# Kernel optimization log

Hardware: AMD Instinct MI355X
Metric: run time of the kernel (lower is better)

Reference implementation:

```python
import jax, jax.numpy as jnp
import numpy as np

K_STEPS = 10
ALPHA = 0.9
N_NODES = 16384
N_CLASSES = 64
N_EDGES = 524288


def setup_inputs() -> dict:
    key = jax.random.key(0)
    k1, k2, k3 = jax.random.split(key, 3)
    masked_y_true = jax.random.normal(k1, (N_NODES, N_CLASSES), dtype=jnp.float32)
    K = jax.random.normal(k2, (N_NODES, N_NODES), dtype=jnp.float32)
    edge_index = jax.random.randint(k3, (2, N_EDGES), 0, N_NODES, dtype=jnp.int32)
    return {"masked_y_true": masked_y_true, "K": K, "edge_index": edge_index}


def reference(masked_y_true, K, edge_index):
    src, dst = edge_index[0], edge_index[1]
    # DAD normalization: w_e = deg(src)^-1/2 * deg(dst)^-1/2
    deg = jnp.zeros((N_NODES,), jnp.float32).at[dst].add(1.0)
    dinv = jax.lax.rsqrt(jnp.maximum(deg, 1.0))
    w = dinv[src] * dinv[dst]  # [E]

    def spmm(x):
        # A @ x with A in edge-list form (static sparsity, reused each step)
        return jax.ops.segment_sum(w[:, None] * x[src], dst, num_segments=N_NODES)

    def prop_step(_, y):
        return ALPHA * spmm(y) + (1.0 - ALPHA) * y

    y = jax.lax.fori_loop(0, K_STEPS, prop_step, masked_y_true)
    y = K @ y
    y = jax.lax.fori_loop(0, K_STEPS, prop_step, y)
    return y
```

## Files before the change

### kernel.cpp

```cpp
#include <hip/hip_runtime.h>

#define NN 16384
#define NC 64
#define NE 524288
#define ALPHA 0.9f
#define KSTEPS 10

typedef _Float16 f16;
typedef _Float16 f16x4 __attribute__((ext_vector_type(4)));
typedef _Float16 f16x8 __attribute__((ext_vector_type(8)));
typedef float f32x4 __attribute__((ext_vector_type(4)));
typedef int i32x16 __attribute__((ext_vector_type(16)));

#define MEMB   asm volatile("" ::: "memory")
#define SCHED0 __builtin_amdgcn_sched_barrier(0)

__global__ __launch_bounds__(256) void deg_kernel(const int* __restrict__ dst,
                                                  unsigned* __restrict__ deg) {
    int e = blockIdx.x * 256 + threadIdx.x;
    atomicAdd(&deg[dst[e]], 1u);
}

__global__ __launch_bounds__(1024) void scan_kernel(const unsigned* __restrict__ deg,
                                                    float* __restrict__ dinv,
                                                    unsigned* __restrict__ rowoff,
                                                    unsigned* __restrict__ cursor) {
    __shared__ unsigned part[1024];
    const int t = threadIdx.x;
    const int base = t * 16;
    unsigned local[16];
    unsigned s = 0;
    #pragma unroll
    for (int i = 0; i < 16; ++i) {
        local[i] = s;
        s += (deg[base + i] + 15u) & ~15u;
    }
    part[t] = s;
    __syncthreads();
    for (int off = 1; off < 1024; off <<= 1) {
        unsigned v = (t >= off) ? part[t - off] : 0u;
        __syncthreads();
        part[t] += v;
        __syncthreads();
    }
    const unsigned ex = (t == 0) ? 0u : part[t - 1];
    #pragma unroll
    for (int i = 0; i < 16; ++i) {
        unsigned ro = ex + local[i];
        rowoff[base + i] = ro;
        cursor[base + i] = ro;
        unsigned d = deg[base + i];
        dinv[base + i] = rsqrtf(fmaxf((float)d, 1.0f));
    }
    if (t == 1023) rowoff[NN] = part[1023];
}

__global__ __launch_bounds__(256) void fill_kernel(const int* __restrict__ src,
                                                   const int* __restrict__ dst,
                                                   const float* __restrict__ dinv,
                                                   unsigned* __restrict__ cursor,
                                                   int2* __restrict__ csr) {
    int e = blockIdx.x * 256 + threadIdx.x;
    int s = src[e], d = dst[e];
    float w = dinv[s] * dinv[d];
    unsigned p = atomicAdd(&cursor[d], 1u);
    csr[p] = make_int2(s, __float_as_int(w));
}

__global__ __launch_bounds__(256) void prop_kernel(const float* __restrict__ x,
                                                   float* __restrict__ y,
                                                   const unsigned* __restrict__ rowoff,
                                                   const int* __restrict__ csr) {
    const int lane = threadIdx.x & 63;
    const int bid = blockIdx.x;
    const int n = __builtin_amdgcn_readfirstlane(((bid & 7) << 11) + ((bid >> 3) << 2)
                                                 + (threadIdx.x >> 6));
    const unsigned beg = rowoff[n];
    const unsigned np = (rowoff[n + 1] - beg) >> 4;
    float acc0 = 0.f, acc1 = 0.f;
    if (np) {
        i32x16 e0 = *(const i32x16*)(csr + 2 * beg);
        i32x16 e1 = *(const i32x16*)(csr + 2 * beg + 16);
        float xv0[8], xv1[8];
        #pragma unroll
        for (int j = 0; j < 8; ++j) xv0[j] = x[(unsigned)e0[2 * j] * 64u + lane];
        #pragma unroll
        for (int j = 0; j < 8; ++j) xv1[j] = x[(unsigned)e1[2 * j] * 64u + lane];
        for (unsigned p = 1; p < np; ++p) {
            const i32x16 f0 = *(const i32x16*)(csr + 2 * (beg + p * 16));
            const i32x16 f1 = *(const i32x16*)(csr + 2 * (beg + p * 16) + 16);
            #pragma unroll
            for (int j = 0; j < 8; ++j) {
                const float w = __int_as_float(e0[2 * j + 1]);
                if (j & 1) acc1 = fmaf(w, xv0[j], acc1);
                else       acc0 = fmaf(w, xv0[j], acc0);
            }
            #pragma unroll
            for (int j = 0; j < 8; ++j) xv0[j] = x[(unsigned)f0[2 * j] * 64u + lane];
            #pragma unroll
            for (int j = 0; j < 8; ++j) {
                const float w = __int_as_float(e1[2 * j + 1]);
                if (j & 1) acc1 = fmaf(w, xv1[j], acc1);
                else       acc0 = fmaf(w, xv1[j], acc0);
            }
            #pragma unroll
            for (int j = 0; j < 8; ++j) xv1[j] = x[(unsigned)f1[2 * j] * 64u + lane];
            e0 = f0; e1 = f1;
        }
        #pragma unroll
        for (int j = 0; j < 8; ++j) {
            const float w = __int_as_float(e0[2 * j + 1]);
            if (j & 1) acc1 = fmaf(w, xv0[j], acc1);
            else       acc0 = fmaf(w, xv0[j], acc0);
        }
        #pragma unroll
        for (int j = 0; j < 8; ++j) {
            const float w = __int_as_float(e1[2 * j + 1]);
            if (j & 1) acc1 = fmaf(w, xv1[j], acc1);
            else       acc0 = fmaf(w, xv1[j], acc0);
        }
    }
    y[n * 64 + lane] = ALPHA * (acc0 + acc1) + (1.0f - ALPHA) * x[n * 64 + lane];
}

__global__ __launch_bounds__(256) void ysplit_kernel(const float* __restrict__ y,
                                                     f16* __restrict__ yhT,
                                                     f16* __restrict__ ylT) {
    __shared__ f16 hb[64][72];
    __shared__ f16 lb[64][72];
    const int t = threadIdx.x;
    const int b = blockIdx.x;
    const int kl = t >> 2;
    const int cq = (t & 3) * 16;
    #pragma unroll
    for (int i = 0; i < 4; ++i) {
        float4 v = *(const float4*)&y[(size_t)(b * 64 + kl) * 64 + cq + i * 4];
        float vv[4] = {v.x, v.y, v.z, v.w};
        #pragma unroll
        for (int j = 0; j < 4; ++j) {
            int c = cq + i * 4 + j;
            f16 h = (f16)vv[j];
            float r = vv[j] - (float)h;
            hb[c][kl] = h;
            lb[c][kl] = (f16)r;
        }
    }
    __syncthreads();
    const int c = t >> 2;
    const int kq = (t & 3) * 16;
    #pragma unroll
    for (int s2 = 0; s2 < 2; ++s2) {
        int slot = (kq >> 3) + s2;
        int dslot = slot ^ (c & 7);
        f16x8 hv, lv;
        #pragma unroll
        for (int j = 0; j < 8; ++j) { hv[j] = hb[c][kq + s2 * 8 + j]; lv[j] = lb[c][kq + s2 * 8 + j]; }
        *(f16x8*)&yhT[(size_t)c * NN + b * 64 + dslot * 8] = hv;
        *(f16x8*)&ylT[(size_t)c * NN + b * 64 + dslot * 8] = lv;
    }
}

__device__ inline void gload16(const void* g, void* l) {
    __builtin_amdgcn_global_load_lds((const __attribute__((address_space(1))) void*)g,
                                     (__attribute__((address_space(3))) void*)l, 16, 0, 0);
}

#define AH_OFF 0
#define AL_OFF 16384
#define YP_OFF 32768

template <bool SLAB>
__global__ __launch_bounds__(256, 2) void gemm_kernel(const float* __restrict__ A,
                                                      const f16* __restrict__ yhT,
                                                      const f16* __restrict__ ylT,
                                                      float* __restrict__ z) {
    __shared__ char lds[65536];
    const int t = threadIdx.x;
    const int w = t >> 6;
    const int l = t & 63;
    const size_t row0 = (size_t)blockIdx.x * 128;
    const int kbase = blockIdx.y * 2048;
    const int stag = (blockIdx.x + blockIdx.y * 4) & 31;

    f32x4 acc[2][4];
    #pragma unroll
    for (int m = 0; m < 2; ++m)
        #pragma unroll
        for (int n = 0; n < 4; ++n)
            acc[m][n] = (f32x4){0.f, 0.f, 0.f, 0.f};

    const int arow_l = w * 4 + (l >> 4);
    const int acol = (l & 15) * 4;
    const int ycr = l >> 3;
    const int yco = (l & 7) * 8;

    float4 aA[8], aB[8];

    auto tmap = [&](int tile) { return (stag + tile) & 31; };

    auto loadA = [&](float4 (&dst)[8], int tile) {
        const int kt = kbase + tmap(tile) * 64;
        #pragma unroll
        for (int i = 0; i < 8; ++i)
            dst[i] = *(const float4*)&A[(row0 + i * 16 + arow_l) * 16384 + kt + acol];
    };
    auto issueY = [&](int tile, int cur) {
        const int kt = kbase + tmap(tile) * 64;
        #pragma unroll
        for (int j = 0; j < 2; ++j) {
            const int i = 2 * w + j;
            gload16(yhT + (size_t)(i * 8 + ycr) * NN + kt + yco,
                    lds + YP_OFF + cur * 16384 + i * 1024);
            gload16(ylT + (size_t)(i * 8 + ycr) * NN + kt + yco,
                    lds + YP_OFF + cur * 16384 + 8192 + i * 1024);
        }
    };
    auto writeA = [&](const float4 (&src)[8]) {
        #pragma unroll
        for (int i = 0; i < 8; ++i) {
            const int r = i * 16 + arow_l;
            float v[4] = {src[i].x, src[i].y, src[i].z, src[i].w};
            f16x4 h4, l4;
            #pragma unroll
            for (int j = 0; j < 4; ++j) {
                f16 h = (f16)v[j];
                h4[j] = h;
                l4[j] = (f16)(v[j] - (float)h);
            }
            const int byte = r * 128 + (((((l & 15) >> 1)) ^ (r & 7)) << 4) + (l & 1) * 8;
            *(f16x4*)(lds + AH_OFF + byte) = h4;
            *(f16x4*)(lds + AL_OFF + byte) = l4;
        }
    };
    auto mfmaTile = [&](int cur) {
        #pragma unroll
        for (int s = 0; s < 2; ++s) {
            const int slot = s * 4 + (l >> 4);
            f16x8 ah[2], alo[2];
            #pragma unroll
            for (int m = 0; m < 2; ++m) {
                const int r = w * 32 + m * 16 + (l & 15);
                const int byte = r * 128 + ((slot ^ (r & 7)) << 4);
                ah[m]  = *(const f16x8*)(lds + AH_OFF + byte);
                alo[m] = *(const f16x8*)(lds + AL_OFF + byte);
            }
            #pragma unroll
            for (int n = 0; n < 4; ++n) {
                const int c = n * 16 + (l & 15);
                const int byte = c * 128 + ((slot ^ (c & 7)) << 4);
                const f16x8 bh = *(const f16x8*)(lds + YP_OFF + cur * 16384 + byte);
                const f16x8 bl = *(const f16x8*)(lds + YP_OFF + cur * 16384 + 8192 + byte);
                #pragma unroll
                for (int m = 0; m < 2; ++m) {
                    acc[m][n] = __builtin_amdgcn_mfma_f32_16x16x32_f16(ah[m],  bh, acc[m][n], 0, 0, 0);
                    acc[m][n] = __builtin_amdgcn_mfma_f32_16x16x32_f16(ah[m],  bl, acc[m][n], 0, 0, 0);
                    acc[m][n] = __builtin_amdgcn_mfma_f32_16x16x32_f16(alo[m], bh, acc[m][n], 0, 0, 0);
                }
            }
        }
    };

    loadA(aA, 0); MEMB;
    issueY(0, 0); MEMB;
    loadA(aB, 1); MEMB;
    writeA(aA);
    asm volatile("s_waitcnt vmcnt(8)" ::: "memory");  SCHED0;
    asm volatile("s_waitcnt lgkmcnt(0)" ::: "memory"); SCHED0;
    __builtin_amdgcn_s_barrier(); SCHED0;

#define GEMM_ITER(TILE, CUR, SETF, SETW)                                      \
    issueY((TILE) + 1, (CUR) ^ 1); MEMB;                                      \
    loadA(SETF, (TILE) + 2); MEMB;                                            \
    mfmaTile(CUR);                                                            \
    MEMB; SCHED0;                                                             \
    __builtin_amdgcn_s_barrier();                 \
    writeA(SETW);                                  \
    asm volatile("s_waitcnt vmcnt(8)" ::: "memory");  SCHED0;   \
    asm volatile("s_waitcnt lgkmcnt(0)" ::: "memory"); SCHED0;                \
    __builtin_amdgcn_s_barrier(); SCHED0;

    for (int tp = 0; tp < 15; ++tp) {
        const int t0 = 2 * tp;
        GEMM_ITER(t0,     0, aA, aB);
        GEMM_ITER(t0 + 1, 1, aB, aA);
    }
    issueY(31, 1); MEMB;
    mfmaTile(0);
    MEMB; SCHED0;
    __builtin_amdgcn_s_barrier();
    writeA(aB);
    asm volatile("s_waitcnt vmcnt(0)" ::: "memory");  SCHED0;
    asm volatile("s_waitcnt lgkmcnt(0)" ::: "memory"); SCHED0;
    __builtin_amdgcn_s_barrier(); SCHED0;
    mfmaTile(1);
#undef GEMM_ITER

    float* zo = SLAB ? (z + (size_t)blockIdx.y * NN * NC) : z;
    #pragma unroll
    for (int m = 0; m < 2; ++m)
        #pragma unroll
        for (int n = 0; n < 4; ++n)
            #pragma unroll
            for (int q = 0; q < 4; ++q) {
                const size_t gr = row0 + w * 32 + m * 16 + (l >> 4) * 4 + q;
                const int gc = n * 16 + (l & 15);
                if (SLAB) zo[gr * 64 + gc] = acc[m][n][q];
                else      atomicAdd(&zo[gr * 64 + gc], acc[m][n][q]);
            }
}

__global__ __launch_bounds__(256) void zred_kernel(const float* __restrict__ zs,
                                                   float* __restrict__ z) {
    const size_t i = ((size_t)blockIdx.x * 256 + threadIdx.x) * 4;
    float4 s = *(const float4*)(zs + i);
    #pragma unroll
    for (int k = 1; k < 8; ++k) {
        const float4 v = *(const float4*)(zs + (size_t)k * NN * NC + i);
        s.x += v.x; s.y += v.y; s.z += v.z; s.w += v.w;
    }
    *(float4*)(z + i) = s;
}

extern "C" void kernel_launch(void* const* d_in, const int* in_sizes, int n_in,
                              void* d_out, int out_size, void* d_ws, size_t ws_size,
                              hipStream_t stream) {
    const float* ytrue = (const float*)d_in[0];
    const float* Kmat  = (const float*)d_in[1];
    const int*   eidx  = (const int*)d_in[2];
    const int* esrc = eidx;
    const int* edst = eidx + NE;
    float* out = (float*)d_out;

    char* ws = (char*)d_ws;
    size_t off = 0;
    auto alloc = [&](size_t bytes) -> void* {
        void* p = ws + off;
        off += (bytes + 255) & ~(size_t)255;
        return p;
    };
    const size_t CSR_ENTRIES = (size_t)NE + 16 * NN;
    unsigned* deg    = (unsigned*)alloc((size_t)NN * 4);
    unsigned* rowoff = (unsigned*)alloc((size_t)(NN + 1) * 4);
    unsigned* cursor = (unsigned*)alloc((size_t)NN * 4);
    float*    dinv   = (float*)alloc((size_t)NN * 4);
    int2*     csr    = (int2*)alloc(CSR_ENTRIES * 8);
    float*    yA     = (float*)alloc((size_t)NN * NC * 4);
    float*    yB     = (float*)alloc((size_t)NN * NC * 4);
    f16*      yhT    = (f16*)alloc((size_t)NC * NN * 2);
    f16*      ylT    = (f16*)alloc((size_t)NC * NN * 2);
    float*    zs     = (float*)alloc((size_t)8 * NN * NC * 4);
    const bool slab_ok = (off <= ws_size);

    hipMemsetAsync(deg, 0, (size_t)NN * 4, stream);
    hipMemsetAsync(csr, 0, CSR_ENTRIES * 8, stream);
    deg_kernel<<<NE / 256, 256, 0, stream>>>(edst, deg);
    scan_kernel<<<1, 1024, 0, stream>>>(deg, dinv, rowoff, cursor);
    fill_kernel<<<NE / 256, 256, 0, stream>>>(esrc, edst, dinv, cursor, csr);

    const float* cur = ytrue;
    float* bufs[2] = {yA, yB};
    int pb = 0;
    for (int s = 0; s < KSTEPS; ++s) {
        float* nxt = bufs[pb];
        pb ^= 1;
        prop_kernel<<<NN / 4, 256, 0, stream>>>(cur, nxt, rowoff, (const int*)csr);
        cur = nxt;
    }

    ysplit_kernel<<<NN / 64, 256, 0, stream>>>(cur, yhT, ylT);

    float* z = (cur == yA) ? yB : yA;
    if (slab_ok) {
        gemm_kernel<true><<<dim3(128, 8), 256, 0, stream>>>(Kmat, yhT, ylT, zs);
        zred_kernel<<<NN * NC / 1024, 256, 0, stream>>>(zs, z);
    } else {
        hipMemsetAsync(z, 0, (size_t)NN * NC * 4, stream);
        gemm_kernel<false><<<dim3(128, 8), 256, 0, stream>>>(Kmat, yhT, ylT, z);
    }

    float* other = (z == yA) ? yB : yA;
    const float* c2 = z;
    for (int s = 0; s < KSTEPS; ++s) {
        float* nxt = (s == KSTEPS - 1) ? out : other;
        prop_kernel<<<NN / 4, 256, 0, stream>>>(c2, nxt, rowoff, (const int*)csr);
        other = (float*)c2;
        c2 = nxt;
    }
}
```

Baseline: 521.9 us.

## Halve GEMM K-tile to 32 to cut LDS and double occupancy

Shrinks the per-iteration K tile of the split-fp16 GEMM from 64 to 32, halving the shared memory buffer to 32 KB and the A prefetch registers. Launch bounds go from 2 to 4 blocks per CU, the LDS swizzle is rewritten for 64-byte rows, and the transposed y layout now stores unswizzled with the XOR applied at load time instead. The aim is more resident waves to hide global-load latency, at the cost of twice as many barriers and loop iterations per block.

Measured after the change: 545.4 us. 1.04x slower.

```diff
diff --git a/kernel.cpp b/kernel.cpp
--- a/kernel.cpp
+++ b/kernel.cpp
@@ -150,13 +150,11 @@
     const int kq = (t & 3) * 16;
     #pragma unroll
     for (int s2 = 0; s2 < 2; ++s2) {
-        int slot = (kq >> 3) + s2;
-        int dslot = slot ^ (c & 7);
         f16x8 hv, lv;
         #pragma unroll
         for (int j = 0; j < 8; ++j) { hv[j] = hb[c][kq + s2 * 8 + j]; lv[j] = lb[c][kq + s2 * 8 + j]; }
-        *(f16x8*)&yhT[(size_t)c * NN + b * 64 + dslot * 8] = hv;
-        *(f16x8*)&ylT[(size_t)c * NN + b * 64 + dslot * 8] = lv;
+        *(f16x8*)&yhT[(size_t)c * NN + b * 64 + kq + s2 * 8] = hv;
+        *(f16x8*)&ylT[(size_t)c * NN + b * 64 + kq + s2 * 8] = lv;
     }
 }
 
@@ -166,21 +164,21 @@
 }
 
 #define AH_OFF 0
-#define AL_OFF 16384
-#define YP_OFF 32768
+#define AL_OFF 8192
+#define YP_OFF 16384
 
 template <bool SLAB>
-__global__ __launch_bounds__(256, 2) void gemm_kernel(const float* __restrict__ A,
+__global__ __launch_bounds__(256, 4) void gemm_kernel(const float* __restrict__ A,
                                                       const f16* __restrict__ yhT,
                                                       const f16* __restrict__ ylT,
                                                       float* __restrict__ z) {
-    __shared__ char lds[65536];
+    __shared__ char lds[32768];
     const int t = threadIdx.x;
     const int w = t >> 6;
     const int l = t & 63;
     const size_t row0 = (size_t)blockIdx.x * 128;
     const int kbase = blockIdx.y * 2048;
-    const int stag = (blockIdx.x + blockIdx.y * 4) & 31;
+    const int stag = (blockIdx.x + blockIdx.y * 4) & 63;
 
     f32x4 acc[2][4];
     #pragma unroll
@@ -189,36 +187,35 @@
         for (int n = 0; n < 4; ++n)
             acc[m][n] = (f32x4){0.f, 0.f, 0.f, 0.f};
 
-    const int arow_l = w * 4 + (l >> 4);
-    const int acol = (l & 15) * 4;
-    const int ycr = l >> 3;
-    const int yco = (l & 7) * 8;
-
-    float4 aA[8], aB[8];
-
-    auto tmap = [&](int tile) { return (stag + tile) & 31; };
-
-    auto loadA = [&](float4 (&dst)[8], int tile) {
-        const int kt = kbase + tmap(tile) * 64;
-        #pragma unroll
-        for (int i = 0; i < 8; ++i)
-            dst[i] = *(const float4*)&A[(row0 + i * 16 + arow_l) * 16384 + kt + acol];
+    const int sar = w * 8 + (l >> 3);
+    const int sac = (l & 7) * 4;
+    const int saslot = (l & 7) >> 1;
+    const int sasub = (l & 7) & 1;
+    const int yc = w * 16 + (l >> 2);
+    const int ysl = (l & 3) ^ (yc & 3);
+
+    float4 aA[4], aB[4];
+
+    auto tmap = [&](int tile) { return (stag + tile) & 63; };
+
+    auto loadA = [&](float4 (&dst)[4], int tile) {
+        const int kt = kbase + tmap(tile) * 32;
+        #pragma unroll
+        for (int i = 0; i < 4; ++i)
+            dst[i] = *(const float4*)&A[(row0 + i * 32 + sar) * 16384 + kt + sac];
     };
     auto issueY = [&](int tile, int cur) {
-        const int kt = kbase + tmap(tile) * 64;
-        #pragma unroll
-        for (int j = 0; j < 2; ++j) {
-            const int i = 2 * w + j;
-            gload16(yhT + (size_t)(i * 8 + ycr) * NN + kt + yco,
-                    lds + YP_OFF + cur * 16384 + i * 1024);
-            gload16(ylT + (size_t)(i * 8 + ycr) * NN + kt + yco,
-                    lds + YP_OFF + cur * 16384 + 8192 + i * 1024);
-        }
-    };
-    auto writeA = [&](const float4 (&src)[8]) {
-        #pragma unroll
-        for (int i = 0; i < 8; ++i) {
-            const int r = i * 16 + arow_l;
+        const int kt = kbase + tmap(tile) * 32;
+        gload16(yhT + (size_t)yc * NN + kt + ysl * 8,
+                lds + YP_OFF + cur * 8192 + w * 1024);
+        gload16(ylT + (size_t)yc * NN + kt + ysl * 8,
+                lds + YP_OFF + cur * 8192 + 4096 + w * 1024);
+    };
+    auto writeA = [&](const float4 (&src)[4]) {
+        #pragma unroll
+        for (int i = 0; i < 4; ++i) {
+            const int r = i * 32 + sar;
+            const int byte = r * 64 + ((saslot ^ (r & 3)) << 4) + sasub * 8;
             float v[4] = {src[i].x, src[i].y, src[i].z, src[i].w};
             f16x4 h4, l4;
             #pragma unroll
@@ -227,35 +224,30 @@
                 h4[j] = h;
                 l4[j] = (f16)(v[j] - (float)h);
             }
-            const int byte = r * 128 + (((((l & 15) >> 1)) ^ (r & 7)) << 4) + (l & 1) * 8;
             *(f16x4*)(lds + AH_OFF + byte) = h4;
             *(f16x4*)(lds + AL_OFF + byte) = l4;
         }
     };
     auto mfmaTile = [&](int cur) {
-        #pragma unroll
-        for (int s = 0; s < 2; ++s) {
-            const int slot = s * 4 + (l >> 4);
-            f16x8 ah[2], alo[2];
+        f16x8 ah[2], alo[2];
+        #pragma unroll
+        for (int m = 0; m < 2; ++m) {
+            const int r = w * 32 + m * 16 + (l & 15);
+            const int byte = r * 64 + (((l >> 4) ^ (r & 3)) << 4);
+            ah[m]  = *(const f16x8*)(lds + AH_OFF + byte);
+            alo[m] = *(const f16x8*)(lds + AL_OFF + byte);
+        }
+        #pragma unroll
+        for (int n = 0; n < 4; ++n) {
+            const int c = n * 16 + (l & 15);
+            const int byte = c * 64 + (((l >> 4) ^ (c & 3)) << 4);
+            const f16x8 bh = *(const f16x8*)(lds + YP_OFF + cur * 8192 + byte);
+            const f16x8 bl = *(const f16x8*)(lds + YP_OFF + cur * 8192 + 4096 + byte);
             #pragma unroll
             for (int m = 0; m < 2; ++m) {
-                const int r = w * 32 + m * 16 + (l & 15);
-                const int byte = r * 128 + ((slot ^ (r & 7)) << 4);
-                ah[m]  = *(const f16x8*)(lds + AH_OFF + byte);
-                alo[m] = *(const f16x8*)(lds + AL_OFF + byte);
-            }
-            #pragma unroll
-            for (int n = 0; n < 4; ++n) {
-                const int c = n * 16 + (l & 15);
-                const int byte = c * 128 + ((slot ^ (c & 7)) << 4);
-                const f16x8 bh = *(const f16x8*)(lds + YP_OFF + cur * 16384 + byte);
-                const f16x8 bl = *(const f16x8*)(lds + YP_OFF + cur * 16384 + 8192 + byte);
-                #pragma unroll
-                for (int m = 0; m < 2; ++m) {
-                    acc[m][n] = __builtin_amdgcn_mfma_f32_16x16x32_f16(ah[m],  bh, acc[m][n], 0, 0, 0);
-                    acc[m][n] = __builtin_amdgcn_mfma_f32_16x16x32_f16(ah[m],  bl, acc[m][n], 0, 0, 0);
-                    acc[m][n] = __builtin_amdgcn_mfma_f32_16x16x32_f16(alo[m], bh, acc[m][n], 0, 0, 0);
-                }
+                acc[m][n] = __builtin_amdgcn_mfma_f32_16x16x32_f16(ah[m],  bh, acc[m][n], 0, 0, 0);
+                acc[m][n] = __builtin_amdgcn_mfma_f32_16x16x32_f16(ah[m],  bl, acc[m][n], 0, 0, 0);
+                acc[m][n] = __builtin_amdgcn_mfma_f32_16x16x32_f16(alo[m], bh, acc[m][n], 0, 0, 0);
             }
         }
     };
@@ -264,7 +256,7 @@
     issueY(0, 0); MEMB;
     loadA(aB, 1); MEMB;
     writeA(aA);
-    asm volatile("s_waitcnt vmcnt(8)" ::: "memory");  SCHED0;
+    asm volatile("s_waitcnt vmcnt(4)" ::: "memory");  SCHED0;
     asm volatile("s_waitcnt lgkmcnt(0)" ::: "memory"); SCHED0;
     __builtin_amdgcn_s_barrier(); SCHED0;
 
@@ -274,17 +266,17 @@
     mfmaTile(CUR);                                                            \
     MEMB; SCHED0;                                                             \
     __builtin_amdgcn_s_barrier();                 \
-    writeA(SETW);                                  \
-    asm volatile("s_waitcnt vmcnt(8)" ::: "memory");  SCHED0;   \
+    writeA(SETW);                                      \
+    asm volatile("s_waitcnt vmcnt(4)" ::: "memory");  SCHED0;   \
     asm volatile("s_waitcnt lgkmcnt(0)" ::: "memory"); SCHED0;                \
     __builtin_amdgcn_s_barrier(); SCHED0;
 
-    for (int tp = 0; tp < 15; ++tp) {
+    for (int tp = 0; tp < 31; ++tp) {
         const int t0 = 2 * tp;
         GEMM_ITER(t0,     0, aA, aB);
         GEMM_ITER(t0 + 1, 1, aB, aA);
     }
-    issueY(31, 1); MEMB;
+    issueY(63, 1); MEMB;
     mfmaTile(0);
     MEMB; SCHED0;
     __builtin_amdgcn_s_barrier();
```
